# Performance work log

Hardware: AMD Instinct MI355X
Metric: run time of the kernel (lower is better)

## Reference

```python
import jax, jax.numpy as jnp
import numpy as np

N_NODES = 48758  # hardcoded in the original DAN.forward
EPS_BN = 1e-5


def setup_inputs() -> dict:
    key = jax.random.key(0)
    ks = jax.random.split(key, 14)
    E, D, R, L, NI = 780000, 128, 4, 2, 10000
    sc = 1.0 / np.sqrt(D)
    inp = {
        "x": jax.random.normal(ks[0], (N_NODES, D), jnp.float32),
        "edge_index": jax.random.randint(ks[1], (2, E), 0, N_NODES),
        "idx": jax.random.randint(ks[2], (NI,), 0, N_NODES),
        "edge_type": jax.random.randint(ks[3], (E,), 0, R),
        "edge_weight": jax.random.uniform(ks[4], (E,), jnp.float32),
        # RiskGNN params
        "proj_w": jax.random.normal(ks[5], (D, D), jnp.float32) * sc,
        "proj_b": jax.random.normal(ks[6], (D,), jnp.float32) * 0.01,
        "bn_g": jnp.ones((D,), jnp.float32),
        "bn_b": jnp.zeros((D,), jnp.float32),
        # per-layer DAN params, stacked over L=2 layers (same dims)
        "win_w": jax.random.normal(ks[7], (L, D, D), jnp.float32) * sc,
        "win_b": jax.random.normal(ks[8], (L, D), jnp.float32) * 0.01,
        "wrel": jax.random.normal(ks[9], (L, R, D, D), jnp.float32) * sc,
        "out_w": jax.random.normal(ks[10], (L, D, D), jnp.float32) * sc,
        "out_b": jax.random.normal(ks[11], (L, D), jnp.float32) * 0.01,
    }
    return inp


def _dan_layer(h, edge_index, edge_type, rel_num, win_w, win_b, wrel, out_w, out_b):
    dst = edge_index[0]
    src = edge_index[1]
    x = h @ win_w + win_b                       # [N, D]
    x_j = x[src]                                # edge gather [E, D]
    # gcn_norm(add_self_loops=False): deg over col (=src axis edge_index[1])
    ones_e = jnp.ones(dst.shape[0], x.dtype)
    deg = jax.ops.segment_sum(ones_e, src, num_segments=N_NODES)
    dinv = jnp.where(deg > 0, jax.lax.rsqrt(jnp.maximum(deg, 1.0)), 0.0)
    norm_w = (dinv[dst] * dinv[src])[:, None]   # [E, 1]
    msg_gcn = jax.ops.segment_sum(x_j * norm_w, dst, num_segments=N_NODES)
    # per-relation masked matmul (unsorted grouped GEMM)
    res = jnp.zeros_like(x_j)
    for r in range(rel_num):
        res = jnp.where((edge_type == r)[:, None], x_j @ wrel[r], res)
    # segment softmax over edges grouped by dst, per channel
    seg_max = jax.ops.segment_max(res, dst, num_segments=N_NODES)
    ex = jnp.exp(res - seg_max[dst])
    denom = jax.ops.segment_sum(ex, dst, num_segments=N_NODES)
    weig = ex / denom[dst]
    msg = jax.ops.segment_sum(res * weig, dst, num_segments=N_NODES)
    out = (msg_gcn + 0.1 * jax.nn.relu(msg)) @ out_w + out_b
    return out


def reference(x, edge_weight, proj_w, proj_b, bn_g, bn_b, win_w, win_b, wrel,
              out_w, out_b, edge_index, edge_type, idx):
    rel_num = wrel.shape[1]
    n_layer = win_w.shape[0]
    h = x @ proj_w + proj_b
    # BatchNorm1d (training-mode batch stats, biased var)
    mu = jnp.mean(h, axis=0)
    var = jnp.mean((h - mu) ** 2, axis=0)
    h = (h - mu) * jax.lax.rsqrt(var + EPS_BN) * bn_g + bn_b
    h = jax.nn.relu(h)
    for i in range(n_layer):
        h = _dan_layer(h, edge_index, edge_type, rel_num,
                       win_w[i], win_b[i], wrel[i], out_w[i], out_b[i])
    h = jax.nn.gelu(h, approximate=False)  # dropout is identity at eval
    return h[idx]
```

## Files before the change

### kernel.cpp

```cpp
#include <hip/hip_runtime.h>
#include <hip/hip_bf16.h>
#include <math.h>

#define D 128
#define DD (128 * 128)
#define RS 640
#define CAPB 4608

typedef __attribute__((ext_vector_type(8))) short short8;
typedef __attribute__((ext_vector_type(4))) float f32x4;

__device__ __forceinline__ float bf2f(unsigned short u) {
    union { unsigned int i; float f; } x; x.i = ((unsigned int)u) << 16; return x.f;
}
__device__ __forceinline__ unsigned short f2bf(float f) {
    unsigned int i = __float_as_uint(f);
    unsigned int r = (i + 0x7FFFu + ((i >> 16) & 1u)) >> 16;
    return (unsigned short)r;
}

__device__ __forceinline__ int vote_flag(const unsigned short* __restrict__ x) {
    __shared__ int bad_s;
    if (threadIdx.x == 0) bad_s = 0;
    __syncthreads();
    unsigned int e = (x[threadIdx.x] >> 7) & 0xFFu;
    unsigned long long b = __ballot(e < 100u || e > 140u);
    if ((threadIdx.x & 63) == 0) atomicAdd(&bad_s, __popcll(b));
    __syncthreads();
    return bad_s > 48 ? 1 : 0;
}

__global__ __launch_bounds__(256) void k_stage1(
    const void* __restrict__ xin, unsigned short* __restrict__ xb, int n4, int nbx, int nbw,
    const void* s0, const void* s1, const void* s2, const void* s3,
    const void* s4, const void* s5, const void* s6, const void* s7, const void* s8,
    int o1, int o2, int o3, int o4, int o5, int o6, int o7, int o8,
    int total, unsigned short* __restrict__ wdst,
    const int* __restrict__ ei, const int* __restrict__ et, int E,
    unsigned int* __restrict__ cd_g, unsigned int* __restrict__ cs_g,
    uint2* __restrict__ ebuck, unsigned short* __restrict__ sbuck)
{
    int bx = blockIdx.x, t = threadIdx.x;
    if (bx < nbx) {
        int fl = vote_flag((const unsigned short*)xin);
        int i = bx * 256 + t;
        if (i >= n4) return;
        if (fl) {
            float4 v = ((const float4*)xin)[i];
            uint2 o;
            o.x = (unsigned int)f2bf(v.x) | ((unsigned int)f2bf(v.y) << 16);
            o.y = (unsigned int)f2bf(v.z) | ((unsigned int)f2bf(v.w) << 16);
            ((uint2*)xb)[i] = o;
        } else {
            ((uint2*)xb)[i] = ((const uint2*)xin)[i];
        }
    } else if (bx < nbx + nbw) {
        int fl = vote_flag((const unsigned short*)xin);
        int i = (bx - nbx) * 256 + t;
        if (i >= total) return;
        const void* src; int base;
        if      (i < o1) { src = s0; base = 0;  }
        else if (i < o2) { src = s1; base = o1; }
        else if (i < o3) { src = s2; base = o2; }
        else if (i < o4) { src = s3; base = o3; }
        else if (i < o5) { src = s4; base = o4; }
        else if (i < o6) { src = s5; base = o5; }
        else if (i < o7) { src = s6; base = o6; }
        else if (i < o8) { src = s7; base = o7; }
        else             { src = s8; base = o8; }
        int li = i - base;
        wdst[i] = fl ? f2bf(((const float*)src)[li]) : ((const unsigned short*)src)[li];
    } else {
        __shared__ unsigned int hd[256], hs[256];
        int b = bx - nbx - nbw;
        hd[t] = 0u; hs[t] = 0u;
        unsigned int d8[8], sp8[8];
        __syncthreads();
        int base = b * 2048;
        #pragma unroll
        for (int i = 0; i < 8; ++i) {
            int e = base + t + i * 256;
            if (e < E) {
                unsigned int d = (unsigned int)ei[e];
                unsigned int s = (unsigned int)ei[E + e];
                unsigned int tt = (unsigned int)et[e];
                d8[i] = d; sp8[i] = s | (tt << 16);
                atomicAdd(&hd[d >> 8], 1u);
                atomicAdd(&hs[s >> 8], 1u);
            } else d8[i] = 0xFFFFFFFFu;
        }
        __syncthreads();
        hd[t] = atomicAdd(&cd_g[t], hd[t]);
        hs[t] = atomicAdd(&cs_g[t], hs[t]);
        __syncthreads();
        #pragma unroll
        for (int i = 0; i < 8; ++i) {
            if (d8[i] != 0xFFFFFFFFu) {
                unsigned int bk = d8[i] >> 8;
                unsigned int pos = atomicAdd(&hd[bk], 1u);
                if (pos < (unsigned)CAPB) ebuck[(size_t)bk * CAPB + pos] = make_uint2(d8[i], sp8[i]);
                unsigned int s = sp8[i] & 0xFFFFu;
                unsigned int bk2 = s >> 8;
                unsigned int pos2 = atomicAdd(&hs[bk2], 1u);
                if (pos2 < (unsigned)CAPB) sbuck[(size_t)bk2 * CAPB + pos2] = (unsigned short)s;
            }
        }
    }
}

__device__ __forceinline__ void gemm_core(
    const unsigned short* __restrict__ A, const unsigned short* __restrict__ W,
    unsigned short* As, unsigned short* Wt, f32x4 (&acc)[2][8])
{
    int t = threadIdx.x;
    #pragma unroll
    for (int i = 0; i < 8; ++i) {
        int ch = t + i * 256;
        int row = ch >> 4;
        int kc  = ch & 15;
        uint4 v = *((const uint4*)(A + (size_t)row * D + kc * 8));
        *((uint4*)&As[row * 128 + (kc ^ (row & 15)) * 8]) = v;
    }
    #pragma unroll
    for (int i = 0; i < 8; ++i) {
        int ch = t + i * 256;
        int k  = ch >> 4;
        int n0 = (ch & 15) * 8;
        uint4 v = *((const uint4*)(W + k * D + n0));
        const unsigned short* pv = (const unsigned short*)&v;
        int kc = k >> 3, ko = k & 7;
        #pragma unroll
        for (int j = 0; j < 8; ++j) {
            int n = n0 + j;
            Wt[n * 128 + ((kc ^ (n & 15)) * 8) + ko] = pv[j];
        }
    }
    __syncthreads();
    int wave = t >> 6, lane = t & 63, quad = lane >> 4, l16 = lane & 15;
    int rowbase = wave * 32;
    #pragma unroll
    for (int a = 0; a < 2; ++a)
        #pragma unroll
        for (int b = 0; b < 8; ++b) acc[a][b] = (f32x4){0.f, 0.f, 0.f, 0.f};
    #pragma unroll
    for (int ks = 0; ks < 4; ++ks) {
        int chunk = ks * 4 + quad;
        short8 af[2], bf[8];
        #pragma unroll
        for (int rt = 0; rt < 2; ++rt) {
            int r = rowbase + rt * 16 + l16;
            af[rt] = *((const short8*)&As[r * 128 + (chunk ^ (r & 15)) * 8]);
        }
        #pragma unroll
        for (int ct = 0; ct < 8; ++ct) {
            int n = ct * 16 + l16;
            bf[ct] = *((const short8*)&Wt[n * 128 + (chunk ^ (n & 15)) * 8]);
        }
        #pragma unroll
        for (int rt = 0; rt < 2; ++rt)
            #pragma unroll
            for (int ct = 0; ct < 8; ++ct)
                acc[rt][ct] = __builtin_amdgcn_mfma_f32_16x16x32_bf16(af[rt], bf[ct], acc[rt][ct], 0, 0, 0);
    }
}

__global__ __launch_bounds__(256) void k_stage2(
    const unsigned int* __restrict__ cd_g, const uint2* __restrict__ ebuck,
    unsigned int* __restrict__ rp, unsigned int* __restrict__ pckd,
    const unsigned int* __restrict__ cs_g, const unsigned short* __restrict__ sbuck,
    float* __restrict__ dinv, int N, int NB,
    const unsigned short* __restrict__ wbase, unsigned short* __restrict__ bc,
    unsigned short* __restrict__ wtg, int o4, int o6, int o7)
{
    __shared__ __align__(16) char pool[65536];
    int bx = blockIdx.x, t = threadIdx.x;
    if (bx < NB) {
        uint2* ebuf = (uint2*)pool;
        unsigned int* bins = (unsigned int*)(pool + CAPB * 8);
        unsigned int* gsum = bins + 1024;
        unsigned int* csc  = gsum + 256;
        int b = bx;
        unsigned int cvt_ = (t < NB) ? min(cd_g[t], (unsigned)CAPB) : 0u;
        csc[t] = cvt_;
        __syncthreads();
        for (int off = 1; off < 256; off <<= 1) {
            unsigned int v = csc[t];
            unsigned int a = (t >= off) ? csc[t - off] : 0u;
            __syncthreads();
            csc[t] = v + a;
            __syncthreads();
        }
        unsigned int cnt = min(cd_g[b], (unsigned)CAPB);
        unsigned int beg = csc[b] - cnt;
        #pragma unroll
        for (int j = 0; j < 4; ++j) bins[t + j * 256] = 0u;
        __syncthreads();
        for (unsigned int i = t; i < cnt; i += 256) {
            uint2 v = ebuck[(size_t)b * CAPB + i];
            ebuf[i] = v;
            atomicAdd(&bins[((v.x & 255u) << 2) | ((v.y >> 16) & 3u)], 1u);
        }
        __syncthreads();
        unsigned int b0 = bins[4 * t], b1 = bins[4 * t + 1], b2 = bins[4 * t + 2], b3 = bins[4 * t + 3];
        unsigned int s4 = b0 + b1 + b2 + b3;
        gsum[t] = s4;
        __syncthreads();
        for (int off = 1; off < 256; off <<= 1) {
            unsigned int v = gsum[t];
            unsigned int a = (t >= off) ? gsum[t - off] : 0u;
            __syncthreads();
            gsum[t] = v + a;
            __syncthreads();
        }
        unsigned int base0 = gsum[t] - s4;
        bins[4 * t]     = beg + base0;
        bins[4 * t + 1] = beg + base0 + b0;
        bins[4 * t + 2] = beg + base0 + b0 + b1;
        bins[4 * t + 3] = beg + base0 + b0 + b1 + b2;
        int n = (b << 8) + t;
        if (n <= N) rp[n] = beg + base0;
        __syncthreads();
        for (unsigned int i = t; i < cnt; i += 256) {
            uint2 v = ebuf[i];
            unsigned int key = ((v.x & 255u) << 2) | ((v.y >> 16) & 3u);
            unsigned int pos = atomicAdd(&bins[key], 1u);
            pckd[pos] = v.y;
        }
    } else if (bx < 2 * NB) {
        unsigned int* bins = (unsigned int*)pool;
        int b = bx - NB;
        unsigned int cnt = min(cs_g[b], (unsigned)CAPB);
        bins[t] = 0u;
        __syncthreads();
        for (unsigned int i = t; i < cnt; i += 256)
            atomicAdd(&bins[sbuck[(size_t)b * CAPB + i] & 255u], 1u);
        __syncthreads();
        int n = (b << 8) + t;
        if (n < N) {
            unsigned int dg = bins[t];
            dinv[n] = dg ? rsqrtf((float)dg) : 0.f;
        }
    } else if (bx < 2 * NB + 8) {
        int cb = bx - 2 * NB;
        int l = cb >> 2;
        const unsigned short* A = wbase + o4 + (size_t)l * DD;
        const unsigned short* W = wbase + o6 + (size_t)cb * DD;
        f32x4 acc[2][8];
        gemm_core(A, W, (unsigned short*)pool, (unsigned short*)pool + DD, acc);
        int wave = t >> 6, lane = t & 63, quad = lane >> 4, l16 = lane & 15;
        int rowbase = wave * 32;
        unsigned short* dst = wtg + (size_t)(3 + cb) * DD;
        #pragma unroll
        for (int rt = 0; rt < 2; ++rt) {
            #pragma unroll
            for (int ct = 0; ct < 8; ++ct) {
                int n = ct * 16 + l16;
                #pragma unroll
                for (int r = 0; r < 4; ++r) {
                    int k = rowbase + rt * 16 + quad * 4 + r;
                    dst[n * 128 + (((k >> 3) ^ (n & 15)) * 8) + (k & 7)] = f2bf(acc[rt][ct][r]);
                }
            }
        }
        const unsigned short* b_in = wbase + o4 + 2 * DD;
        if (t < 128) {
            float s = 0.f;
            for (int k = 0; k < 128; ++k)
                s += bf2f(b_in[l * D + k]) * bf2f(W[k * D + t]);
            bc[cb * D + t] = f2bf(s);
        }
    } else {
        int pb = bx - 2 * NB - 8;
        int mi = pb >> 3, sub = pb & 7;
        const int mmap[5] = {0, 1, 2, 11, 12};
        int m = mmap[mi];
        const unsigned short* src;
        if (mi == 0) src = wbase;
        else if (mi <= 2) src = wbase + o4 + (size_t)(mi - 1) * DD;
        else src = wbase + o7 + (size_t)(mi - 3) * DD;
        int c = sub * 256 + t;
        int n = c >> 4, kc = c & 15;
        unsigned short tmp[8];
        #pragma unroll
        for (int ko = 0; ko < 8; ++ko) tmp[ko] = src[(kc * 8 + ko) * 128 + n];
        *((uint4*)(wtg + (size_t)m * DD + n * 128 + ((kc ^ (n & 15)) * 8))) = *(uint4*)tmp;
    }
}

__device__ __forceinline__ void load_afrag(
    const unsigned short* __restrict__ A, int M, int blockRow, short8 (&af)[2][4])
{
    int t = threadIdx.x;
    int wave = t >> 6, lane = t & 63, quad = lane >> 4, l16 = lane & 15;
    int rowbase = blockRow + wave * 32;
    int r0 = min(rowbase + l16, M - 1);
    int r1 = min(rowbase + 16 + l16, M - 1);
    const unsigned short* a0 = A + (size_t)r0 * D;
    const unsigned short* a1 = A + (size_t)r1 * D;
    #pragma unroll
    for (int ks = 0; ks < 4; ++ks) {
        int chunk = ks * 4 + quad;
        af[0][ks] = *((const short8*)(a0 + chunk * 8));
        af[1][ks] = *((const short8*)(a1 + chunk * 8));
    }
}

__device__ __forceinline__ void mfma_slice(
    const unsigned short* Wt, short8 (&af)[2][4], f32x4 (&acc)[2][8])
{
    int lane = threadIdx.x & 63, quad = lane >> 4, l16 = lane & 15;
    #pragma unroll
    for (int a = 0; a < 2; ++a)
        #pragma unroll
        for (int b = 0; b < 8; ++b) acc[a][b] = (f32x4){0.f, 0.f, 0.f, 0.f};
    #pragma unroll
    for (int ks = 0; ks < 4; ++ks) {
        int chunk = ks * 4 + quad;
        short8 bf[8];
        #pragma unroll
        for (int ct = 0; ct < 8; ++ct)
            bf[ct] = *((const short8*)&Wt[(ct * 16 + l16) * 128 + ((chunk ^ l16) * 8)]);
        #pragma unroll
        for (int rt = 0; rt < 2; ++rt)
            #pragma unroll
            for (int ct = 0; ct < 8; ++ct)
                acc[rt][ct] = __builtin_amdgcn_mfma_f32_16x16x32_bf16(af[rt][ks], bf[ct], acc[rt][ct], 0, 0, 0);
    }
}

__device__ __forceinline__ void gemm_core_fast(
    const unsigned short* __restrict__ A, const unsigned short* __restrict__ Wt_g,
    int M, int blockRow, unsigned short* Wt, f32x4 (&acc)[2][8])
{
    int t = threadIdx.x;
    #pragma unroll
    for (int i = 0; i < 8; ++i)
        ((uint4*)Wt)[t + i * 256] = ((const uint4*)Wt_g)[t + i * 256];
    short8 af[2][4];
    load_afrag(A, M, blockRow, af);
    __syncthreads();
    mfma_slice(Wt, af, acc);
}

__device__ __forceinline__ void store_c(
    f32x4 (&acc)[2][8], const unsigned short* __restrict__ bias,
    unsigned short* __restrict__ C, int M, int blockRow, int ldc, int coloff)
{
    int t = threadIdx.x;
    int wave = t >> 6, lane = t & 63, quad = lane >> 4, l16 = lane & 15;
    int rowbase = wave * 32;
    #pragma unroll
    for (int rt = 0; rt < 2; ++rt) {
        #pragma unroll
        for (int ct = 0; ct < 8; ++ct) {
            int col = ct * 16 + l16;
            float bv = bias ? bf2f(bias[col]) : 0.f;
            #pragma unroll
            for (int r = 0; r < 4; ++r) {
                int grow = blockRow + rowbase + rt * 16 + quad * 4 + r;
                if (grow < M) {
                    float v = acc[rt][ct][r] + bv;
                    C[(size_t)grow * ldc + coloff + col] = f2bf(v);
                }
            }
        }
    }
}

__global__ __launch_bounds__(256) void gemm_fast(
    const unsigned short* __restrict__ A, const unsigned short* __restrict__ Wt_g,
    const unsigned short* __restrict__ bias, unsigned short* __restrict__ C, int M)
{
    __shared__ unsigned short Wt[DD];
    f32x4 acc[2][8];
    gemm_core_fast(A, Wt_g, M, blockIdx.x * 128, Wt, acc);
    store_c(acc, bias, C, M, blockIdx.x * 128, D, 0);
}

__global__ __launch_bounds__(256) void gemm_proj(
    const unsigned short* __restrict__ A, const unsigned short* __restrict__ Wt_g,
    const unsigned short* __restrict__ bias, unsigned short* __restrict__ C,
    int M, float* __restrict__ psum, float* __restrict__ psq)
{
    __shared__ unsigned short Wt[DD];
    __shared__ float smS[4][128], smQ[4][128];
    f32x4 acc[2][8];
    int blockRow = blockIdx.x * 128;
    gemm_core_fast(A, Wt_g, M, blockRow, Wt, acc);
    int t = threadIdx.x;
    int wave = t >> 6, lane = t & 63, quad = lane >> 4, l16 = lane & 15;
    int rowbase = wave * 32;
    #pragma unroll
    for (int ct = 0; ct < 8; ++ct) {
        int col = ct * 16 + l16;
        float bv = bf2f(bias[col]);
        float ps = 0.f, pq = 0.f;
        #pragma unroll
        for (int rt = 0; rt < 2; ++rt) {
            #pragma unroll
            for (int r = 0; r < 4; ++r) {
                int grow = blockRow + rowbase + rt * 16 + quad * 4 + r;
                if (grow < M) {
                    float v = acc[rt][ct][r] + bv;
                    C[(size_t)grow * D + col] = f2bf(v);
                    ps += v; pq += v * v;
                }
            }
        }
        ps += __shfl_xor(ps, 16, 64); ps += __shfl_xor(ps, 32, 64);
        pq += __shfl_xor(pq, 16, 64); pq += __shfl_xor(pq, 32, 64);
        if (quad == 0) { smS[wave][col] = ps; smQ[wave][col] = pq; }
    }
    __syncthreads();
    if (t < 128) {
        psum[blockIdx.x * 128 + t] = smS[0][t] + smS[1][t] + smS[2][t] + smS[3][t];
        psq[blockIdx.x * 128 + t]  = smQ[0][t] + smQ[1][t] + smQ[2][t] + smQ[3][t];
    }
}

__global__ void k_bnstats(const float* __restrict__ psum, const float* __restrict__ psq,
                          int nb, int N, const unsigned short* __restrict__ g,
                          const unsigned short* __restrict__ b,
                          float* __restrict__ scale, float* __restrict__ shift) {
    int col = threadIdx.x & 127, h = threadIdx.x >> 7;
    float s = 0.f, q = 0.f;
    for (int i = h; i < nb; i += 2) { s += psum[i * 128 + col]; q += psq[i * 128 + col]; }
    __shared__ float sS[256], sQ[256];
    sS[threadIdx.x] = s; sQ[threadIdx.x] = q;
    __syncthreads();
    if (h == 0) {
        s = sS[col] + sS[col + 128];
        q = sQ[col] + sQ[col + 128];
        float inv = 1.f / (float)N;
        float mean = s * inv;
        float var = fmaxf(q * inv - mean * mean, 0.f);
        float sc = rsqrtf(var + 1e-5f) * bf2f(g[col]);
        scale[col] = sc;
        shift[col] = bf2f(b[col]) - mean * sc;
    }
}

__global__ __launch_bounds__(256) void gemm_fused(
    const unsigned short* __restrict__ h, const unsigned short* __restrict__ wtg,
    const unsigned short* __restrict__ b_in_l, const unsigned short* __restrict__ bc_l,
    unsigned char* __restrict__ xy8, const float* __restrict__ dinv,
    const float* __restrict__ bnsc, const float* __restrict__ bnsh, int M, int l)
{
    __shared__ unsigned short Wt[DD];
    f32x4 acc[2][8];
    int slice = blockIdx.y;
    int m = (slice == 0) ? (1 + l) : (3 + l * 4 + slice - 1);
    int blockRow = blockIdx.x * 128;
    int t = threadIdx.x;
    const unsigned short* Wt_g = wtg + (size_t)m * DD;
    #pragma unroll
    for (int i = 0; i < 8; ++i)
        ((uint4*)Wt)[t + i * 256] = ((const uint4*)Wt_g)[t + i * 256];
    short8 af[2][4];
    load_afrag(h, M, blockRow, af);
    if (bnsc) {
        int quad = (t & 63) >> 4;
        #pragma unroll
        for (int rt = 0; rt < 2; ++rt)
            #pragma unroll
            for (int ks = 0; ks < 4; ++ks) {
                int ch0 = (ks * 4 + quad) * 8;
                unsigned short* p = (unsigned short*)&af[rt][ks];
                #pragma unroll
                for (int j = 0; j < 8; ++j) {
                    float f = bf2f(p[j]);
                    f = fmaxf(fmaf(f, bnsc[ch0 + j], bnsh[ch0 + j]), 0.f);
                    p[j] = f2bf(f);
                }
            }
    }
    __syncthreads();
    mfma_slice(Wt, af, acc);

    int wave = t >> 6, lane = t & 63, quad = lane >> 4, l16 = lane & 15;
    int rowbase = wave * 32;
    int boff = (slice == 0) ? 0 : (128 + (slice - 1) * 128);
    #pragma unroll
    for (int rt = 0; rt < 2; ++rt) {
        float dv[4];
        if (slice == 0) {
            #pragma unroll
            for (int r = 0; r < 4; ++r) {
                int grow = min(blockRow + rowbase + rt * 16 + quad * 4 + r, M - 1);
                dv[r] = dinv[grow];
            }
        }
        #pragma unroll
        for (int ct = 0; ct < 8; ++ct) {
            int col = ct * 16 + l16;
            float bv = (slice == 0) ? bf2f(b_in_l[col]) : bf2f(bc_l[(slice - 1) * D + col]);
            #pragma unroll
            for (int r = 0; r < 4; ++r) {
                int grow = blockRow + rowbase + rt * 16 + quad * 4 + r;
                if (grow < M) {
                    float v = acc[rt][ct][r] + bv;
                    if (slice == 0) v *= dv[r];
                    int p = __builtin_amdgcn_cvt_pk_fp8_f32(v, v, 0, false);
                    xy8[(size_t)grow * RS + boff + col] = (unsigned char)(p & 0xFF);
                }
            }
        }
    }
}

__global__ __launch_bounds__(256) void gemm_out(
    const unsigned short* __restrict__ zg, const unsigned short* __restrict__ Wt_g,
    const unsigned short* __restrict__ bias, void* __restrict__ out,
    int M, const unsigned short* __restrict__ xprobe)
{
    int fl = vote_flag(xprobe);
    __shared__ unsigned short Wt[DD];
    f32x4 acc[2][8];
    int blockRow = blockIdx.x * 128;
    gemm_core_fast(zg, Wt_g, M, blockRow, Wt, acc);
    int t = threadIdx.x;
    int wave = t >> 6, lane = t & 63, quad = lane >> 4, l16 = lane & 15;
    int rowbase = wave * 32;
    #pragma unroll
    for (int rt = 0; rt < 2; ++rt) {
        #pragma unroll
        for (int ct = 0; ct < 8; ++ct) {
            int col = ct * 16 + l16;
            float bv = bf2f(bias[col]);
            #pragma unroll
            for (int r = 0; r < 4; ++r) {
                int grow = blockRow + rowbase + rt * 16 + quad * 4 + r;
                if (grow < M) {
                    float v = acc[rt][ct][r] + bv;
                    float gl = 0.5f * v * (1.f + erff(v * 0.70710678118654752f));
                    size_t o = (size_t)grow * D + col;
                    if (fl) ((float*)out)[o] = gl;
                    else    ((unsigned short*)out)[o] = f2bf(gl);
                }
            }
        }
    }
}

__device__ __forceinline__ void acc_edge2(uint2 xv, uint2 yv, float vm,
                                          float* g, float* dd, float* ss) {
    const unsigned int* xw = (const unsigned int*)&xv;
    const unsigned int* yw = (const unsigned int*)&yv;
    #pragma unroll
    for (int w = 0; w < 2; ++w) {
        auto xlo = __builtin_amdgcn_cvt_pk_f32_fp8(xw[w], false);
        auto xhi = __builtin_amdgcn_cvt_pk_f32_fp8(xw[w], true);
        auto ylo = __builtin_amdgcn_cvt_pk_f32_fp8(yw[w], false);
        auto yhi = __builtin_amdgcn_cvt_pk_f32_fp8(yw[w], true);
        float vx[4] = {xlo[0], xlo[1], xhi[0], xhi[1]};
        float vy[4] = {ylo[0], ylo[1], yhi[0], yhi[1]};
        int j = 4 * w;
        #pragma unroll
        for (int i = 0; i < 4; ++i) {
            g[j + i] = fmaf(vx[i], vm, g[j + i]);
            float e = __expf(vy[i]);
            dd[j + i] = fmaf(e, vm, dd[j + i]);
            ss[j + i] = fmaf(vy[i] * e, vm, ss[j + i]);
        }
    }
}

__global__ __launch_bounds__(256) void k_edge(
    const unsigned int* __restrict__ rp, const unsigned int* __restrict__ packed,
    const unsigned char* __restrict__ xy8, const float* __restrict__ dinv,
    unsigned short* __restrict__ zout, int NN, const int* __restrict__ nodes)
{
    int lane = threadIdx.x & 63;
    int slot = blockIdx.x * 4 + (threadIdx.x >> 6);
    if (slot >= NN) return;
    int node = nodes ? nodes[slot] : slot;
    node = __builtin_amdgcn_readfirstlane(node);
    unsigned int beg = rp[node], end = rp[node + 1];
    int eg = lane >> 4;
    int cb = (lane & 15) * 8;
    float g[8], dd[8], ss[8];
    #pragma unroll
    for (int j = 0; j < 8; ++j) { g[j] = 0.f; dd[j] = 0.f; ss[j] = 0.f; }

    for (unsigned int e0 = beg; e0 < end; e0 += 8) {
        unsigned int eA = e0 + (unsigned int)eg;
        unsigned int eB = eA + 4u;
        float vmA = (eA < end) ? 1.f : 0.f;
        float vmB = (eB < end) ? 1.f : 0.f;
        unsigned int pA = packed[(eA < end) ? eA : beg];
        unsigned int pB = packed[(eB < end) ? eB : beg];
        unsigned int sA = pA & 0xFFFFu, tA = (pA >> 16) & 3u;
        unsigned int sB = pB & 0xFFFFu, tB = (pB >> 16) & 3u;
        const unsigned char* bA = xy8 + (size_t)sA * RS;
        const unsigned char* bB = xy8 + (size_t)sB * RS;
        uint2 xvA = *((const uint2*)(bA + cb));
        uint2 yvA = *((const uint2*)(bA + 128 + tA * 128 + cb));
        uint2 xvB = *((const uint2*)(bB + cb));
        uint2 yvB = *((const uint2*)(bB + 128 + tB * 128 + cb));
        acc_edge2(xvA, yvA, vmA, g, dd, ss);
        acc_edge2(xvB, yvB, vmB, g, dd, ss);
    }

    #pragma unroll
    for (int j = 0; j < 8; ++j) {
        g[j]  += __shfl_xor(g[j], 16, 64);  g[j]  += __shfl_xor(g[j], 32, 64);
        dd[j] += __shfl_xor(dd[j], 16, 64); dd[j] += __shfl_xor(dd[j], 32, 64);
        ss[j] += __shfl_xor(ss[j], 16, 64); ss[j] += __shfl_xor(ss[j], 32, 64);
    }
    if (eg == 0) {
        float dn = dinv[node];
        unsigned int o[4];
        #pragma unroll
        for (int w = 0; w < 4; ++w) {
            int j0 = w * 2, j1 = w * 2 + 1;
            float m0 = (dd[j0] > 0.f) ? ss[j0] / dd[j0] : 0.f;
            float m1 = (dd[j1] > 0.f) ? ss[j1] / dd[j1] : 0.f;
            float z0 = fmaf(g[j0], dn, 0.1f * fmaxf(m0, 0.f));
            float z1 = fmaf(g[j1], dn, 0.1f * fmaxf(m1, 0.f));
            o[w] = (unsigned int)f2bf(z0) | ((unsigned int)f2bf(z1) << 16);
        }
        *((uint4*)(zout + (size_t)slot * D + cb)) = *(uint4*)o;
    }
}

extern "C" void kernel_launch(void* const* d_in, const int* in_sizes, int n_in,
                              void* d_out, int out_size, void* d_ws, size_t ws_size,
                              hipStream_t stream)
{
    const int* ei  = (const int*)d_in[1];
    const int* idx = (const int*)d_in[2];
    const int* et  = (const int*)d_in[3];
    const unsigned short* xprobe = (const unsigned short*)d_in[0];

    int N  = in_sizes[0] / D;
    int E  = in_sizes[1] / 2;
    int NI = in_sizes[2];
    int L  = in_sizes[9] / (D * D);
    int R  = in_sizes[11] / (L * D * D);

    int NB = (N + 255) >> 8;
    int BA = (E + 2047) / 2048;

    char* ws = (char*)d_ws;
    size_t off = 0;
    auto alloc = [&](size_t bytes) -> char* {
        char* p = ws + off;
        off += (bytes + 255) & ~(size_t)255;
        return p;
    };
    unsigned short* h    = (unsigned short*)alloc((size_t)N * D * 2);
    unsigned char*  xy8  = (unsigned char*)alloc((size_t)N * RS);
    unsigned short* z    = (unsigned short*)alloc((size_t)N * D * 2);
    unsigned short* xb   = (unsigned short*)alloc((size_t)N * D * 2);
    unsigned short* zg   = (unsigned short*)alloc((size_t)NI * D * 2);
    float*          dinv = (float*)alloc((size_t)N * 4);
    unsigned int*   rp   = (unsigned int*)alloc((size_t)(N + 1) * 4);
    unsigned int*   pckd = (unsigned int*)alloc((size_t)E * 4);
    int gb  = (N + 127) / 128;
    float*          psum = (float*)alloc((size_t)gb * 128 * 4);
    float*          psq  = (float*)alloc((size_t)gb * 128 * 4);
    float*          bscale = (float*)alloc(128 * 4);
    float*          bshift = (float*)alloc(128 * 4);
    unsigned int*   cursors = (unsigned int*)alloc(512 * 4);
    unsigned int*   cd_g = cursors;
    unsigned int*   cs_g = cursors + 256;
    uint2*          ebuck = (uint2*)xy8;
    unsigned short* sbuck = (unsigned short*)z;
    int o1 = D * D;
    int o2 = o1 + D;
    int o3 = o2 + D;
    int o4 = o3 + D;
    int o5 = o4 + L * D * D;
    int o6 = o5 + L * D;
    int o7 = o6 + L * R * D * D;
    int o8 = o7 + L * D * D;
    int wt = o8 + L * D;
    unsigned short* wbase  = (unsigned short*)alloc((size_t)wt * 2);
    unsigned short* b_proj = wbase + o1;
    unsigned short* g_bn   = wbase + o2;
    unsigned short* b_bn   = wbase + o3;
    unsigned short* b_in   = wbase + o5;
    unsigned short* b_out  = wbase + o8;
    unsigned short* bc     = (unsigned short*)alloc((size_t)L * R * D * 2);
    unsigned short* wtg    = (unsigned short*)alloc((size_t)13 * DD * 2);
    (void)ws_size; (void)n_in; (void)out_size;

    int gb2 = (NI + 127) / 128;
    int nb4 = (N + 3) / 4;
    int ni4 = (NI + 3) / 4;
    int n4 = N * D / 4;
    int nbx = (n4 + 255) / 256;
    int nbw = (wt + 255) / 256;

    hipMemsetAsync(cursors, 0, 512 * 4, stream);

    k_stage1<<<nbx + nbw + BA, 256, 0, stream>>>(
        d_in[0], xb, n4, nbx, nbw,
        d_in[5], d_in[6], d_in[7], d_in[8], d_in[9], d_in[10], d_in[11], d_in[12], d_in[13],
        o1, o2, o3, o4, o5, o6, o7, o8, wt, wbase,
        ei, et, E, cd_g, cs_g, ebuck, sbuck);

    k_stage2<<<2 * NB + 8 + 40, 256, 0, stream>>>(
        cd_g, ebuck, rp, pckd, cs_g, sbuck, dinv, N, NB,
        wbase, bc, wtg, o4, o6, o7);

    gemm_proj<<<gb, 256, 0, stream>>>(xb, wtg, b_proj, h, N, psum, psq);
    k_bnstats<<<1, 256, 0, stream>>>(psum, psq, gb, N, g_bn, b_bn, bscale, bshift);

    gemm_fused<<<dim3(gb, 1 + R), 256, 0, stream>>>(h, wtg, b_in, bc, xy8, dinv, bscale, bshift, N, 0);
    k_edge<<<nb4, 256, 0, stream>>>(rp, pckd, xy8, dinv, z, N, nullptr);
    gemm_fast<<<gb, 256, 0, stream>>>(z, wtg + (size_t)11 * DD, b_out, h, N);

    gemm_fused<<<dim3(gb, 1 + R), 256, 0, stream>>>(h, wtg, b_in + D, bc + R * D, xy8, dinv, nullptr, nullptr, N, 1);
    k_edge<<<ni4, 256, 0, stream>>>(rp, pckd, xy8, dinv, zg, NI, idx);

    gemm_out<<<gb2, 256, 0, stream>>>(zg, wtg + (size_t)12 * DD, b_out + D, d_out, NI, xprobe);
}
```

Measured before the change: 364.7 us.

## Fold layer-0 output projection into layer-1 input weights and parallelize BN stats

```diff
diff --git a/kernel.cpp b/kernel.cpp
--- a/kernel.cpp
+++ b/kernel.cpp
@@ -164,13 +164,33 @@
     }
 }
 
+__device__ __forceinline__ void store_transposed(f32x4 (&acc)[2][8], unsigned short* dst)
+{
+    int t = threadIdx.x;
+    int wave = t >> 6, lane = t & 63, quad = lane >> 4, l16 = lane & 15;
+    int rowbase = wave * 32;
+    #pragma unroll
+    for (int rt = 0; rt < 2; ++rt) {
+        #pragma unroll
+        for (int ct = 0; ct < 8; ++ct) {
+            int n = ct * 16 + l16;
+            #pragma unroll
+            for (int r = 0; r < 4; ++r) {
+                int k = rowbase + rt * 16 + quad * 4 + r;
+                dst[n * 128 + (((k >> 3) ^ (n & 15)) * 8) + (k & 7)] = f2bf(acc[rt][ct][r]);
+            }
+        }
+    }
+}
+
 __global__ __launch_bounds__(256) void k_stage2(
     const unsigned int* __restrict__ cd_g, const uint2* __restrict__ ebuck,
     unsigned int* __restrict__ rp, unsigned int* __restrict__ pckd,
     const unsigned int* __restrict__ cs_g, const unsigned short* __restrict__ sbuck,
     float* __restrict__ dinv, int N, int NB,
     const unsigned short* __restrict__ wbase, unsigned short* __restrict__ bc,
-    unsigned short* __restrict__ wtg, int o4, int o6, int o7)
+    unsigned short* __restrict__ wtg, unsigned short* __restrict__ wraw,
+    unsigned short* __restrict__ bxl1, int o4, int o5, int o6, int o7, int o8)
 {
     __shared__ __align__(16) char pool[65536];
     int bx = blockIdx.x, t = threadIdx.x;
@@ -240,50 +260,80 @@
             unsigned int dg = bins[t];
             dinv[n] = dg ? rsqrtf((float)dg) : 0.f;
         }
-    } else if (bx < 2 * NB + 8) {
-        int cb = bx - 2 * NB;
-        int l = cb >> 2;
-        const unsigned short* A = wbase + o4 + (size_t)l * DD;
-        const unsigned short* W = wbase + o6 + (size_t)cb * DD;
+    } else if (bx < 2 * NB + 4) {
+        int r = bx - 2 * NB;
+        const unsigned short* A = wbase + o4;
+        const unsigned short* W = wbase + o6 + (size_t)r * DD;
         f32x4 acc[2][8];
         gemm_core(A, W, (unsigned short*)pool, (unsigned short*)pool + DD, acc);
-        int wave = t >> 6, lane = t & 63, quad = lane >> 4, l16 = lane & 15;
-        int rowbase = wave * 32;
-        unsigned short* dst = wtg + (size_t)(3 + cb) * DD;
-        #pragma unroll
-        for (int rt = 0; rt < 2; ++rt) {
-            #pragma unroll
-            for (int ct = 0; ct < 8; ++ct) {
-                int n = ct * 16 + l16;
-                #pragma unroll
-                for (int r = 0; r < 4; ++r) {
-                    int k = rowbase + rt * 16 + quad * 4 + r;
-                    dst[n * 128 + (((k >> 3) ^ (n & 15)) * 8) + (k & 7)] = f2bf(acc[rt][ct][r]);
-                }
-            }
-        }
-        const unsigned short* b_in = wbase + o4 + 2 * DD;
+        store_transposed(acc, wtg + (size_t)(3 + r) * DD);
+        const unsigned short* b_in0 = wbase + o5;
         if (t < 128) {
             float s = 0.f;
             for (int k = 0; k < 128; ++k)
-                s += bf2f(b_in[l * D + k]) * bf2f(W[k * D + t]);
-            bc[cb * D + t] = f2bf(s);
+                s += bf2f(b_in0[k]) * bf2f(W[k * D + t]);
+            bc[r * D + t] = f2bf(s);
+        }
+    } else if (bx == 2 * NB + 4) {
+        const unsigned short* A = wbase + o7;
+        const unsigned short* W = wbase + o4 + DD;
+        f32x4 acc[2][8];
+        gemm_core(A, W, (unsigned short*)pool, (unsigned short*)pool + DD, acc);
+        store_transposed(acc, wtg + (size_t)2 * DD);
+        int wave = t >> 6, lane = t & 63, quad = lane >> 4, l16 = lane & 15;
+        int rowbase = wave * 32;
+        #pragma unroll
+        for (int rt = 0; rt < 2; ++rt)
+            #pragma unroll
+            for (int ct = 0; ct < 8; ++ct) {
+                int col = ct * 16 + l16;
+                #pragma unroll
+                for (int r = 0; r < 4; ++r) {
+                    int row = rowbase + rt * 16 + quad * 4 + r;
+                    wraw[row * 128 + col] = f2bf(acc[rt][ct][r]);
+                }
+            }
+        const unsigned short* b_out0 = wbase + o8;
+        const unsigned short* b_in1  = wbase + o5 + D;
+        if (t < 128) {
+            float s = bf2f(b_in1[t]);
+            for (int k = 0; k < 128; ++k)
+                s += bf2f(b_out0[k]) * bf2f(W[k * D + t]);
+            bxl1[t] = f2bf(s);
         }
     } else {
-        int pb = bx - 2 * NB - 8;
+        int pb = bx - 2 * NB - 5;
         int mi = pb >> 3, sub = pb & 7;
-        const int mmap[5] = {0, 1, 2, 11, 12};
-        int m = mmap[mi];
         const unsigned short* src;
-        if (mi == 0) src = wbase;
-        else if (mi <= 2) src = wbase + o4 + (size_t)(mi - 1) * DD;
-        else src = wbase + o7 + (size_t)(mi - 3) * DD;
+        int m;
+        if (mi == 0)      { src = wbase;            m = 0;  }
+        else if (mi == 1) { src = wbase + o4;       m = 1;  }
+        else              { src = wbase + o7 + DD;  m = 12; }
         int c = sub * 256 + t;
         int n = c >> 4, kc = c & 15;
         unsigned short tmp[8];
         #pragma unroll
         for (int ko = 0; ko < 8; ++ko) tmp[ko] = src[(kc * 8 + ko) * 128 + n];
         *((uint4*)(wtg + (size_t)m * DD + n * 128 + ((kc ^ (n & 15)) * 8))) = *(uint4*)tmp;
+    }
+}
+
+__global__ __launch_bounds__(256) void k_stage2b(
+    const unsigned short* __restrict__ wraw, const unsigned short* __restrict__ wbase,
+    const unsigned short* __restrict__ bxl1, unsigned short* __restrict__ bc,
+    unsigned short* __restrict__ wtg, int o6)
+{
+    __shared__ __align__(16) unsigned short pool[2 * DD];
+    int r = blockIdx.x, t = threadIdx.x;
+    const unsigned short* W = wbase + o6 + (size_t)(4 + r) * DD;
+    f32x4 acc[2][8];
+    gemm_core(wraw, W, pool, pool + DD, acc);
+    store_transposed(acc, wtg + (size_t)(7 + r) * DD);
+    if (t < 128) {
+        float s = 0.f;
+        for (int k = 0; k < 128; ++k)
+            s += bf2f(bxl1[k]) * bf2f(W[k * D + t]);
+        bc[(4 + r) * D + t] = f2bf(s);
     }
 }
 
@@ -340,41 +390,6 @@
     load_afrag(A, M, blockRow, af);
     __syncthreads();
     mfma_slice(Wt, af, acc);
-}
-
-__device__ __forceinline__ void store_c(
-    f32x4 (&acc)[2][8], const unsigned short* __restrict__ bias,
-    unsigned short* __restrict__ C, int M, int blockRow, int ldc, int coloff)
-{
-    int t = threadIdx.x;
-    int wave = t >> 6, lane = t & 63, quad = lane >> 4, l16 = lane & 15;
-    int rowbase = wave * 32;
-    #pragma unroll
-    for (int rt = 0; rt < 2; ++rt) {
-        #pragma unroll
-        for (int ct = 0; ct < 8; ++ct) {
-            int col = ct * 16 + l16;
-            float bv = bias ? bf2f(bias[col]) : 0.f;
-            #pragma unroll
-            for (int r = 0; r < 4; ++r) {
-                int grow = blockRow + rowbase + rt * 16 + quad * 4 + r;
-                if (grow < M) {
-                    float v = acc[rt][ct][r] + bv;
-                    C[(size_t)grow * ldc + coloff + col] = f2bf(v);
-                }
-            }
-        }
-    }
-}
-
-__global__ __launch_bounds__(256) void gemm_fast(
-    const unsigned short* __restrict__ A, const unsigned short* __restrict__ Wt_g,
-    const unsigned short* __restrict__ bias, unsigned short* __restrict__ C, int M)
-{
-    __shared__ unsigned short Wt[DD];
-    f32x4 acc[2][8];
-    gemm_core_fast(A, Wt_g, M, blockIdx.x * 128, Wt, acc);
-    store_c(acc, bias, C, M, blockIdx.x * 128, D, 0);
 }
 
 __global__ __launch_bounds__(256) void gemm_proj(
@@ -418,19 +433,29 @@
     }
 }
 
-__global__ void k_bnstats(const float* __restrict__ psum, const float* __restrict__ psq,
-                          int nb, int N, const unsigned short* __restrict__ g,
-                          const unsigned short* __restrict__ b,
-                          float* __restrict__ scale, float* __restrict__ shift) {
-    int col = threadIdx.x & 127, h = threadIdx.x >> 7;
+__global__ __launch_bounds__(256) void k_bnstats(
+    const float* __restrict__ psum, const float* __restrict__ psq,
+    int nb, int N, const unsigned short* __restrict__ g,
+    const unsigned short* __restrict__ b,
+    float* __restrict__ scale, float* __restrict__ shift)
+{
+    int col = blockIdx.x, t = threadIdx.x;
     float s = 0.f, q = 0.f;
-    for (int i = h; i < nb; i += 2) { s += psum[i * 128 + col]; q += psq[i * 128 + col]; }
-    __shared__ float sS[256], sQ[256];
-    sS[threadIdx.x] = s; sQ[threadIdx.x] = q;
+    for (int i = t; i < nb; i += 256) {
+        s += psum[i * 128 + col];
+        q += psq[i * 128 + col];
+    }
+    #pragma unroll
+    for (int o = 32; o >= 1; o >>= 1) {
+        s += __shfl_xor(s, o, 64);
+        q += __shfl_xor(q, o, 64);
+    }
+    __shared__ float sS[4], sQ[4];
+    if ((t & 63) == 0) { sS[t >> 6] = s; sQ[t >> 6] = q; }
     __syncthreads();
-    if (h == 0) {
-        s = sS[col] + sS[col + 128];
-        q = sQ[col] + sQ[col + 128];
+    if (t == 0) {
+        s = sS[0] + sS[1] + sS[2] + sS[3];
+        q = sQ[0] + sQ[1] + sQ[2] + sQ[3];
         float inv = 1.f / (float)N;
         float mean = s * inv;
         float var = fmaxf(q * inv - mean * mean, 0.f);
@@ -683,6 +708,8 @@
     unsigned short* b_out  = wbase + o8;
     unsigned short* bc     = (unsigned short*)alloc((size_t)L * R * D * 2);
     unsigned short* wtg    = (unsigned short*)alloc((size_t)13 * DD * 2);
+    unsigned short* wraw   = (unsigned short*)alloc((size_t)DD * 2);
+    unsigned short* bxl1   = (unsigned short*)alloc((size_t)D * 2);
     (void)ws_size; (void)n_in; (void)out_size;
 
     int gb2 = (NI + 127) / 128;
@@ -700,18 +727,19 @@
         o1, o2, o3, o4, o5, o6, o7, o8, wt, wbase,
         ei, et, E, cd_g, cs_g, ebuck, sbuck);
 
-    k_stage2<<<2 * NB + 8 + 40, 256, 0, stream>>>(
+    k_stage2<<<2 * NB + 5 + 24, 256, 0, stream>>>(
         cd_g, ebuck, rp, pckd, cs_g, sbuck, dinv, N, NB,
-        wbase, bc, wtg, o4, o6, o7);
+        wbase, bc, wtg, wraw, bxl1, o4, o5, o6, o7, o8);
+
+    k_stage2b<<<R, 256, 0, stream>>>(wraw, wbase, bxl1, bc, wtg, o6);
 
     gemm_proj<<<gb, 256, 0, stream>>>(xb, wtg, b_proj, h, N, psum, psq);
-    k_bnstats<<<1, 256, 0, stream>>>(psum, psq, gb, N, g_bn, b_bn, bscale, bshift);
+    k_bnstats<<<128, 256, 0, stream>>>(psum, psq, gb, N, g_bn, b_bn, bscale, bshift);
 
     gemm_fused<<<dim3(gb, 1 + R), 256, 0, stream>>>(h, wtg, b_in, bc, xy8, dinv, bscale, bshift, N, 0);
     k_edge<<<nb4, 256, 0, stream>>>(rp, pckd, xy8, dinv, z, N, nullptr);
-    gemm_fast<<<gb, 256, 0, stream>>>(z, wtg + (size_t)11 * DD, b_out, h, N);
-
-    gemm_fused<<<dim3(gb, 1 + R), 256, 0, stream>>>(h, wtg, b_in + D, bc + R * D, xy8, dinv, nullptr, nullptr, N, 1);
+
+    gemm_fused<<<dim3(gb, 1 + R), 256, 0, stream>>>(z, wtg, bxl1, bc + R * D, xy8, dinv, nullptr, nullptr, N, 1);
     k_edge<<<ni4, 256, 0, stream>>>(rp, pckd, xy8, dinv, zg, NI, idx);
 
     gemm_out<<<gb2, 256, 0, stream>>>(zg, wtg + (size_t)12 * DD, b_out + D, d_out, NI, xprobe);
```

Result: faster. 313.5 us (-14.0%).
